# Performance work log

Measured on AMD Instinct MI355X. Metric: run time of the kernel, lower is better.

## Reference

```python
import jax, jax.numpy as jnp
import numpy as np

# Module config (from init_kwargs): causal=False, window_size=(256,256), window_type=0,
# softmax_scale=None -> 1/sqrt(D), dropout=0 (eval mode).
WINDOW_LEFT, WINDOW_RIGHT = 256, 256


def _window_mask(Sq, Sk, causal, use_window_mask):
    """Boolean [Sq, Sk] visibility mask, FA2 semantics (right-aligned offset)."""
    qi = jnp.arange(Sq)[:, None]
    kj = jnp.arange(Sk)[None, :]
    offset = Sk - Sq
    if causal:
        return kj <= qi + offset  # window (-1, 0)
    if use_window_mask:
        m = jnp.ones((Sq, Sk), dtype=bool)
        if WINDOW_LEFT >= 0:
            m = m & (kj >= qi + offset - WINDOW_LEFT)
        if WINDOW_RIGHT >= 0:
            m = m & (kj <= qi + offset + WINDOW_RIGHT)
        return m
    return None  # full attention


def setup_inputs() -> dict:
    key = jax.random.key(0)
    kq, kkv = jax.random.split(key)
    B, Sq, Sk, H, D = 2, 2048, 2048, 16, 64
    q = jax.random.normal(kq, (B, Sq, H, D), dtype=jnp.float32)
    kv = jax.random.normal(kkv, (B, Sk, 2, H, D), dtype=jnp.float32)
    return {"q": q, "kv": kv, "causal": 0, "use_window_mask": 1, "return_attn_probs": 0}


def reference(q, kv, causal, use_window_mask, return_attn_probs):
    # q: (B, Sq, H, D); kv: (B, Sk, 2, H, D)
    B, Sq, H, D = q.shape
    Sk = kv.shape[1]
    k = kv[:, :, 0]  # (B, Sk, H, D)
    v = kv[:, :, 1]
    scale = 1.0 / (D ** 0.5)
    scores = jnp.einsum('bqhd,bkhd->bhqk', q, k) * scale  # (B, H, Sq, Sk)
    mask = _window_mask(Sq, Sk, bool(causal), bool(use_window_mask))
    if mask is not None:
        scores = jnp.where(mask[None, None], scores, jnp.finfo(scores.dtype).min)
    probs = jax.nn.softmax(scores, axis=-1)
    out = jnp.einsum('bhqk,bkhd->bqhd', probs, v)  # (B, Sq, H, D)
    return out
```

## Files before the change

kernel.cpp:

```cpp
#include <hip/hip_runtime.h>
#include <hip/hip_bf16.h>

#define B_    2
#define SQ_   2048
#define SK_   2048
#define NH_   16
#define DH_   64
#define WIN_  256
#define NEG_  -30000.0f

typedef __bf16 bf16_t;
typedef bf16_t bf16x8 __attribute__((ext_vector_type(8)));
typedef bf16_t bf16x4 __attribute__((ext_vector_type(4)));
typedef float  f32x4  __attribute__((ext_vector_type(4)));
typedef short  s16x4  __attribute__((ext_vector_type(4)));

#define KSTRIDE 72
#define VSTRIDE 72
#define PSTRIDE 72

#if defined(__has_builtin)
#if __has_builtin(__builtin_amdgcn_mfma_f32_16x16x16bf16_1k)
#define HAVE_MFMA16 1
#endif
#endif

__global__ __launch_bounds__(512, 4)
void fa_fwd(const float* __restrict__ qg, const float* __restrict__ kvg,
            float* __restrict__ outg) {
  const int tid  = threadIdx.x;
  const int wid  = tid >> 6;
  const int lane = tid & 63;
  const int quad = lane >> 4;
  const int li   = lane & 15;

  const int bid = blockIdx.x;
  const int qb  = bid >> 5;
  const int bh  = bid & 31;
  const int b   = bh >> 4;
  const int h   = bh & 15;

  const int q0b = qb * 128;
  const int q0  = q0b + wid * 16;

  __shared__ __align__(16) bf16_t sK [2][64 * KSTRIDE];
  __shared__ __align__(16) bf16_t sVT[2][64 * VSTRIDE];
#ifndef HAVE_MFMA16
  __shared__ __align__(16) bf16_t sP [8][16 * PSTRIDE];
  bf16_t* pl = sP[wid];
#endif

  const float qscale = 0.125f * 1.44269504088896340736f;
  const float* qrow = qg + ((size_t)((b * SQ_ + q0 + li) * NH_ + h)) * DH_;
  bf16x8 qfrag[2];
#pragma unroll
  for (int c = 0; c < 2; ++c) {
    f32x4 a0 = *(const f32x4*)(qrow + c * 32 + quad * 8);
    f32x4 a1 = *(const f32x4*)(qrow + c * 32 + quad * 8 + 4);
#pragma unroll
    for (int i = 0; i < 4; ++i) {
      qfrag[c][i]     = (bf16_t)(a0[i] * qscale);
      qfrag[c][i + 4] = (bf16_t)(a1[i] * qscale);
    }
  }

  f32x4 oacc[4];
#pragma unroll
  for (int t = 0; t < 4; ++t) { f32x4 z = {0.f, 0.f, 0.f, 0.f}; oacc[t] = z; }
  float m = NEG_, l = 0.f;

  int klo = q0b - WIN_; if (klo < 0) klo = 0;
  int khi = q0b + 127 + WIN_ + 1; if (khi > SK_) khi = SK_;

  const float* kbase = kvg + (size_t)b * SK_ * 2 * NH_ * DH_ + (size_t)h * DH_;
  const float* vbase = kbase + NH_ * DH_;
  const size_t krow_stride = 2 * NH_ * DH_;

  const int skey = tid >> 3;
  const int sd0  = (tid & 7) * 8;
  const int vcol = skey ^ (((sd0 >> 3) & 7) << 3);

  f32x4 ka[2], va[2];
  {
    const float* kr = kbase + (size_t)(klo + skey) * krow_stride + sd0;
    const float* vr = vbase + (size_t)(klo + skey) * krow_stride + sd0;
    ka[0] = *(const f32x4*)kr;       ka[1] = *(const f32x4*)(kr + 4);
    va[0] = *(const f32x4*)vr;       va[1] = *(const f32x4*)(vr + 4);
  }
  {
    bf16x8 w;
#pragma unroll
    for (int i = 0; i < 4; ++i) { w[i] = (bf16_t)ka[0][i]; w[i + 4] = (bf16_t)ka[1][i]; }
    *(bf16x8*)(&sK[0][skey * KSTRIDE + sd0]) = w;
#pragma unroll
    for (int i = 0; i < 4; ++i) {
      sVT[0][(sd0 + i)     * VSTRIDE + vcol] = (bf16_t)va[0][i];
      sVT[0][(sd0 + 4 + i) * VSTRIDE + vcol] = (bf16_t)va[1][i];
    }
  }
  __syncthreads();

  int buf = 0;
  for (int kk = klo; kk < khi; kk += 64) {
    const bool nxt = (kk + 64 < khi);
    if (nxt) {
      const float* kr = kbase + (size_t)(kk + 64 + skey) * krow_stride + sd0;
      const float* vr = vbase + (size_t)(kk + 64 + skey) * krow_stride + sd0;
      ka[0] = *(const f32x4*)kr;       ka[1] = *(const f32x4*)(kr + 4);
      va[0] = *(const f32x4*)vr;       va[1] = *(const f32x4*)(vr + 4);
    }

    if (kk + 63 >= q0 - WIN_ && kk <= q0 + 15 + WIN_) {
      f32x4 sc[4];
#pragma unroll
      for (int s = 0; s < 4; ++s) {
        bf16x8 kf0 = *(const bf16x8*)(&sK[buf][(s * 16 + li) * KSTRIDE + quad * 8]);
        bf16x8 kf1 = *(const bf16x8*)(&sK[buf][(s * 16 + li) * KSTRIDE + 32 + quad * 8]);
        f32x4 acc = {0.f, 0.f, 0.f, 0.f};
        acc = __builtin_amdgcn_mfma_f32_16x16x32_bf16(kf0, qfrag[0], acc, 0, 0, 0);
        acc = __builtin_amdgcn_mfma_f32_16x16x32_bf16(kf1, qfrag[1], acc, 0, 0, 0);
        sc[s] = acc;
      }
      if (kk < q0 - 241 || kk > q0 + 193) {
        const int qa = q0 + li;
#pragma unroll
        for (int s = 0; s < 4; ++s)
#pragma unroll
          for (int r = 0; r < 4; ++r) {
            int key = kk + s * 16 + quad * 4 + r;
            unsigned dd = (unsigned)(key - qa + WIN_);
            if (dd > 2u * WIN_) sc[s][r] = NEG_;
          }
      }
      float tmax = NEG_;
#pragma unroll
      for (int s = 0; s < 4; ++s)
        tmax = fmaxf(tmax, fmaxf(fmaxf(sc[s][0], sc[s][1]), fmaxf(sc[s][2], sc[s][3])));
      tmax = fmaxf(tmax, __shfl_xor(tmax, 16));
      tmax = fmaxf(tmax, __shfl_xor(tmax, 32));

      const bool defer = (__all(tmax <= m + 8.0f) != 0);
      const float mnew = defer ? m : fmaxf(m, tmax);

      float psum = 0.f;
#ifdef HAVE_MFMA16
      bf16x4 pa[4];
#pragma unroll
      for (int s = 0; s < 4; ++s) {
        float p0 = exp2f(sc[s][0] - mnew);
        float p1 = exp2f(sc[s][1] - mnew);
        float p2 = exp2f(sc[s][2] - mnew);
        float p3 = exp2f(sc[s][3] - mnew);
        psum += (p0 + p1) + (p2 + p3);
        pa[s][0] = (bf16_t)p0; pa[s][1] = (bf16_t)p1;
        pa[s][2] = (bf16_t)p2; pa[s][3] = (bf16_t)p3;
      }
#else
#pragma unroll
      for (int s = 0; s < 4; ++s) {
        bf16x4 pk;
#pragma unroll
        for (int r = 0; r < 4; ++r) {
          float p = exp2f(sc[s][r] - mnew);
          psum += p;
          pk[r] = (bf16_t)p;
        }
        *(bf16x4*)(&pl[li * PSTRIDE + s * 16 + quad * 4]) = pk;
      }
#endif
      psum += __shfl_xor(psum, 16);
      psum += __shfl_xor(psum, 32);

      if (!defer) {
        const float alpha = exp2f(m - mnew);
        float al[4];
#pragma unroll
        for (int r = 0; r < 4; ++r) al[r] = __shfl(alpha, quad * 4 + r);
#pragma unroll
        for (int t = 0; t < 4; ++t) {
          oacc[t][0] *= al[0]; oacc[t][1] *= al[1];
          oacc[t][2] *= al[2]; oacc[t][3] *= al[3];
        }
        l = l * alpha + psum;
        m = mnew;
      } else {
        l += psum;
      }

#ifdef HAVE_MFMA16
#pragma unroll
      for (int s = 0; s < 4; ++s) {
        const s16x4 pas = __builtin_bit_cast(s16x4, pa[s]);
#pragma unroll
        for (int t = 0; t < 4; ++t) {
          const int d  = 16 * t + li;
          const int c8 = ((2 * t + (li >> 3)) & 7) << 3;
          s16x4 vb = *(const s16x4*)(&sVT[buf][d * VSTRIDE + ((s * 16 + quad * 4) ^ c8)]);
          oacc[t] = __builtin_amdgcn_mfma_f32_16x16x16bf16_1k(pas, vb, oacc[t], 0, 0, 0);
        }
      }
#else
      asm volatile("s_waitcnt lgkmcnt(0)" ::: "memory");
#pragma unroll
      for (int kc = 0; kc < 2; ++kc) {
        bf16x8 pf = *(const bf16x8*)(&pl[li * PSTRIDE + kc * 32 + quad * 8]);
#pragma unroll
        for (int t = 0; t < 4; ++t) {
          const int d = 16 * t + li;
          const int c = ((2 * t + (li >> 3)) & 7) << 3;
          bf16x8 vf = *(const bf16x8*)(&sVT[buf][d * VSTRIDE + ((kc * 32 + quad * 8) ^ c)]);
          oacc[t] = __builtin_amdgcn_mfma_f32_16x16x32_bf16(pf, vf, oacc[t], 0, 0, 0);
        }
      }
#endif
    }

    if (nxt) {
      bf16x8 w;
#pragma unroll
      for (int i = 0; i < 4; ++i) { w[i] = (bf16_t)ka[0][i]; w[i + 4] = (bf16_t)ka[1][i]; }
      *(bf16x8*)(&sK[buf ^ 1][skey * KSTRIDE + sd0]) = w;
#pragma unroll
      for (int i = 0; i < 4; ++i) {
        sVT[buf ^ 1][(sd0 + i)     * VSTRIDE + vcol] = (bf16_t)va[0][i];
        sVT[buf ^ 1][(sd0 + 4 + i) * VSTRIDE + vcol] = (bf16_t)va[1][i];
      }
    }
    __syncthreads();
    buf ^= 1;
  }

  float rl[4];
#pragma unroll
  for (int r = 0; r < 4; ++r) {
    float lv = __shfl(l, quad * 4 + r);
    rl[r] = 1.0f / lv;
  }
  float* orow = outg + ((size_t)((b * SQ_ + q0) * NH_ + h)) * DH_;
#pragma unroll
  for (int t = 0; t < 4; ++t)
#pragma unroll
    for (int r = 0; r < 4; ++r)
      orow[(size_t)(quad * 4 + r) * (NH_ * DH_) + 16 * t + li] = oacc[t][r] * rl[r];
}

extern "C" void kernel_launch(void* const* d_in, const int* in_sizes, int n_in,
                              void* d_out, int out_size, void* d_ws, size_t ws_size,
                              hipStream_t stream) {
  (void)in_sizes; (void)n_in; (void)out_size; (void)d_ws; (void)ws_size;
  const float* q  = (const float*)d_in[0];
  const float* kv = (const float*)d_in[1];
  float* out = (float*)d_out;
  dim3 grid(B_ * NH_ * (SQ_ / 128));
  fa_fwd<<<grid, 512, 0, stream>>>(q, kv, out);
}
```

Before: 113.1 us.

## Shrink query tile to 64 rows and defer row-sum reduction to epilogue

Each block now covers 64 query rows with 4 warps (256 threads) instead of 128 rows with 8 warps, and the grid doubles. The smaller tile cuts the key range each block scans, so fewer 64-key tiles fall outside a warp's window. Each thread now loads 16 K/V elements per tile instead of 8. The row-sum shuffle reduction moves out of the loop to the end, and the row-max shuffle now runs only when the max is not deferred. The unused non-MFMA16 fallback path is removed. In exchange, more blocks reload overlapping K/V windows, which raises global traffic.

```diff
diff --git a/kernel.cpp b/kernel.cpp
--- a/kernel.cpp
+++ b/kernel.cpp
@@ -17,15 +17,8 @@
 
 #define KSTRIDE 72
 #define VSTRIDE 72
-#define PSTRIDE 72
-
-#if defined(__has_builtin)
-#if __has_builtin(__builtin_amdgcn_mfma_f32_16x16x16bf16_1k)
-#define HAVE_MFMA16 1
-#endif
-#endif
-
-__global__ __launch_bounds__(512, 4)
+
+__global__ __launch_bounds__(256, 4)
 void fa_fwd(const float* __restrict__ qg, const float* __restrict__ kvg,
             float* __restrict__ outg) {
   const int tid  = threadIdx.x;
@@ -40,15 +33,11 @@
   const int b   = bh >> 4;
   const int h   = bh & 15;
 
-  const int q0b = qb * 128;
+  const int q0b = qb * 64;
   const int q0  = q0b + wid * 16;
 
   __shared__ __align__(16) bf16_t sK [2][64 * KSTRIDE];
   __shared__ __align__(16) bf16_t sVT[2][64 * VSTRIDE];
-#ifndef HAVE_MFMA16
-  __shared__ __align__(16) bf16_t sP [8][16 * PSTRIDE];
-  bf16_t* pl = sP[wid];
-#endif
 
   const float qscale = 0.125f * 1.44269504088896340736f;
   const float* qrow = qg + ((size_t)((b * SQ_ + q0 + li) * NH_ + h)) * DH_;
@@ -70,32 +59,41 @@
   float m = NEG_, l = 0.f;
 
   int klo = q0b - WIN_; if (klo < 0) klo = 0;
-  int khi = q0b + 127 + WIN_ + 1; if (khi > SK_) khi = SK_;
+  int khi = q0b + 63 + WIN_ + 1; if (khi > SK_) khi = SK_;
 
   const float* kbase = kvg + (size_t)b * SK_ * 2 * NH_ * DH_ + (size_t)h * DH_;
   const float* vbase = kbase + NH_ * DH_;
   const size_t krow_stride = 2 * NH_ * DH_;
 
-  const int skey = tid >> 3;
-  const int sd0  = (tid & 7) * 8;
-  const int vcol = skey ^ (((sd0 >> 3) & 7) << 3);
-
-  f32x4 ka[2], va[2];
+  const int skey = tid >> 2;
+  const int sd0  = (tid & 3) * 16;
+
+  f32x4 ka[4], va[4];
   {
     const float* kr = kbase + (size_t)(klo + skey) * krow_stride + sd0;
     const float* vr = vbase + (size_t)(klo + skey) * krow_stride + sd0;
-    ka[0] = *(const f32x4*)kr;       ka[1] = *(const f32x4*)(kr + 4);
-    va[0] = *(const f32x4*)vr;       va[1] = *(const f32x4*)(vr + 4);
+#pragma unroll
+    for (int i = 0; i < 4; ++i) {
+      ka[i] = *(const f32x4*)(kr + 4 * i);
+      va[i] = *(const f32x4*)(vr + 4 * i);
+    }
   }
   {
-    bf16x8 w;
-#pragma unroll
-    for (int i = 0; i < 4; ++i) { w[i] = (bf16_t)ka[0][i]; w[i + 4] = (bf16_t)ka[1][i]; }
-    *(bf16x8*)(&sK[0][skey * KSTRIDE + sd0]) = w;
-#pragma unroll
-    for (int i = 0; i < 4; ++i) {
-      sVT[0][(sd0 + i)     * VSTRIDE + vcol] = (bf16_t)va[0][i];
-      sVT[0][(sd0 + 4 + i) * VSTRIDE + vcol] = (bf16_t)va[1][i];
+#pragma unroll
+    for (int hh = 0; hh < 2; ++hh) {
+      bf16x8 wk;
+#pragma unroll
+      for (int i = 0; i < 4; ++i) {
+        wk[i] = (bf16_t)ka[2 * hh][i]; wk[i + 4] = (bf16_t)ka[2 * hh + 1][i];
+      }
+      *(bf16x8*)(&sK[0][skey * KSTRIDE + sd0 + 8 * hh]) = wk;
+      const int dbase = sd0 + 8 * hh;
+      const int vcol  = skey ^ (((dbase >> 3) & 7) << 3);
+#pragma unroll
+      for (int i = 0; i < 4; ++i) {
+        sVT[0][(dbase + i)     * VSTRIDE + vcol] = (bf16_t)va[2 * hh][i];
+        sVT[0][(dbase + 4 + i) * VSTRIDE + vcol] = (bf16_t)va[2 * hh + 1][i];
+      }
     }
   }
   __syncthreads();
@@ -106,8 +104,11 @@
     if (nxt) {
       const float* kr = kbase + (size_t)(kk + 64 + skey) * krow_stride + sd0;
       const float* vr = vbase + (size_t)(kk + 64 + skey) * krow_stride + sd0;
-      ka[0] = *(const f32x4*)kr;       ka[1] = *(const f32x4*)(kr + 4);
-      va[0] = *(const f32x4*)vr;       va[1] = *(const f32x4*)(vr + 4);
+#pragma unroll
+      for (int i = 0; i < 4; ++i) {
+        ka[i] = *(const f32x4*)(kr + 4 * i);
+        va[i] = *(const f32x4*)(vr + 4 * i);
+      }
     }
 
     if (kk + 63 >= q0 - WIN_ && kk <= q0 + 15 + WIN_) {
@@ -132,18 +133,20 @@
             if (dd > 2u * WIN_) sc[s][r] = NEG_;
           }
       }
-      float tmax = NEG_;
+      float tl = NEG_;
 #pragma unroll
       for (int s = 0; s < 4; ++s)
-        tmax = fmaxf(tmax, fmaxf(fmaxf(sc[s][0], sc[s][1]), fmaxf(sc[s][2], sc[s][3])));
-      tmax = fmaxf(tmax, __shfl_xor(tmax, 16));
-      tmax = fmaxf(tmax, __shfl_xor(tmax, 32));
-
-      const bool defer = (__all(tmax <= m + 8.0f) != 0);
-      const float mnew = defer ? m : fmaxf(m, tmax);
+        tl = fmaxf(tl, fmaxf(fmaxf(sc[s][0], sc[s][1]), fmaxf(sc[s][2], sc[s][3])));
+
+      const bool defer = (__all(tl <= m + 8.0f) != 0);
+      float mnew = m;
+      if (!defer) {
+        float tr = fmaxf(tl, __shfl_xor(tl, 16));
+        tr = fmaxf(tr, __shfl_xor(tr, 32));
+        mnew = fmaxf(m, tr);
+      }
 
       float psum = 0.f;
-#ifdef HAVE_MFMA16
       bf16x4 pa[4];
 #pragma unroll
       for (int s = 0; s < 4; ++s) {
@@ -155,21 +158,6 @@
         pa[s][0] = (bf16_t)p0; pa[s][1] = (bf16_t)p1;
         pa[s][2] = (bf16_t)p2; pa[s][3] = (bf16_t)p3;
       }
-#else
-#pragma unroll
-      for (int s = 0; s < 4; ++s) {
-        bf16x4 pk;
-#pragma unroll
-        for (int r = 0; r < 4; ++r) {
-          float p = exp2f(sc[s][r] - mnew);
-          psum += p;
-          pk[r] = (bf16_t)p;
-        }
-        *(bf16x4*)(&pl[li * PSTRIDE + s * 16 + quad * 4]) = pk;
-      }
-#endif
-      psum += __shfl_xor(psum, 16);
-      psum += __shfl_xor(psum, 32);
 
       if (!defer) {
         const float alpha = exp2f(m - mnew);
@@ -187,7 +175,6 @@
         l += psum;
       }
 
-#ifdef HAVE_MFMA16
 #pragma unroll
       for (int s = 0; s < 4; ++s) {
         const s16x4 pas = __builtin_bit_cast(s16x4, pa[s]);
@@ -199,37 +186,32 @@
           oacc[t] = __builtin_amdgcn_mfma_f32_16x16x16bf16_1k(pas, vb, oacc[t], 0, 0, 0);
         }
       }
-#else
-      asm volatile("s_waitcnt lgkmcnt(0)" ::: "memory");
-#pragma unroll
-      for (int kc = 0; kc < 2; ++kc) {
-        bf16x8 pf = *(const bf16x8*)(&pl[li * PSTRIDE + kc * 32 + quad * 8]);
-#pragma unroll
-        for (int t = 0; t < 4; ++t) {
-          const int d = 16 * t + li;
-          const int c = ((2 * t + (li >> 3)) & 7) << 3;
-          bf16x8 vf = *(const bf16x8*)(&sVT[buf][d * VSTRIDE + ((kc * 32 + quad * 8) ^ c)]);
-          oacc[t] = __builtin_amdgcn_mfma_f32_16x16x32_bf16(pf, vf, oacc[t], 0, 0, 0);
-        }
-      }
-#endif
     }
 
     if (nxt) {
-      bf16x8 w;
-#pragma unroll
-      for (int i = 0; i < 4; ++i) { w[i] = (bf16_t)ka[0][i]; w[i + 4] = (bf16_t)ka[1][i]; }
-      *(bf16x8*)(&sK[buf ^ 1][skey * KSTRIDE + sd0]) = w;
-#pragma unroll
-      for (int i = 0; i < 4; ++i) {
-        sVT[buf ^ 1][(sd0 + i)     * VSTRIDE + vcol] = (bf16_t)va[0][i];
-        sVT[buf ^ 1][(sd0 + 4 + i) * VSTRIDE + vcol] = (bf16_t)va[1][i];
+#pragma unroll
+      for (int hh = 0; hh < 2; ++hh) {
+        bf16x8 wk;
+#pragma unroll
+        for (int i = 0; i < 4; ++i) {
+          wk[i] = (bf16_t)ka[2 * hh][i]; wk[i + 4] = (bf16_t)ka[2 * hh + 1][i];
+        }
+        *(bf16x8*)(&sK[buf ^ 1][skey * KSTRIDE + sd0 + 8 * hh]) = wk;
+        const int dbase = sd0 + 8 * hh;
+        const int vcol  = skey ^ (((dbase >> 3) & 7) << 3);
+#pragma unroll
+        for (int i = 0; i < 4; ++i) {
+          sVT[buf ^ 1][(dbase + i)     * VSTRIDE + vcol] = (bf16_t)va[2 * hh][i];
+          sVT[buf ^ 1][(dbase + 4 + i) * VSTRIDE + vcol] = (bf16_t)va[2 * hh + 1][i];
+        }
       }
     }
     __syncthreads();
     buf ^= 1;
   }
 
+  l += __shfl_xor(l, 16);
+  l += __shfl_xor(l, 32);
   float rl[4];
 #pragma unroll
   for (int r = 0; r < 4; ++r) {
@@ -251,6 +233,6 @@
   const float* q  = (const float*)d_in[0];
   const float* kv = (const float*)d_in[1];
   float* out = (float*)d_out;
-  dim3 grid(B_ * NH_ * (SQ_ / 128));
-  fa_fwd<<<grid, 512, 0, stream>>>(q, kv, out);
+  dim3 grid(B_ * NH_ * (SQ_ / 64));
+  fa_fwd<<<grid, 256, 0, stream>>>(q, kv, out);
 }
```

Result: slower. 117.9 us (+4.2%).
